# Kernel optimization log

Measured on AMD Instinct MI355X. Metric: run time of the kernel, lower is better.

The kernel has to match this reference:

```python
import jax, jax.numpy as jnp
import numpy as np

K = 12  # kNN neighbors (includes self, as in PyG knn(x, x, k))
EPS = 1e-5


def bn(h, g, b):
    # Training-mode BatchNorm over all axes except the last (feature) axis.
    ax = tuple(range(h.ndim - 1))
    m = h.mean(axis=ax, keepdims=True)
    v = h.var(axis=ax, keepdims=True)  # biased variance, as BN uses
    return g * (h - m) * jax.lax.rsqrt(v + EPS) + b


def edge_conv(x, W1, b1, g, be, W2, b2):
    # x: [B, N, C] -> [B, N, H]. Dynamic kNN graph in feature space per graph.
    d2 = jnp.sum(x * x, axis=-1)                                  # [B, N]
    dist = d2[:, :, None] + d2[:, None, :] - 2.0 * jnp.einsum('bic,bjc->bij', x, x)
    _, idx = jax.lax.top_k(-dist, K)                              # [B, N, K]
    xj = jnp.take_along_axis(x[:, None, :, :], idx[:, :, :, None], axis=2)  # [B,N,K,C]
    xi = jnp.broadcast_to(x[:, :, None, :], xj.shape)
    e = jnp.concatenate([xi, xj - xi], axis=-1)                   # [B,N,K,2C]
    h = jax.nn.relu(bn(jnp.einsum('bnkc,ch->bnkh', e, W1) + b1, g, be))
    h = jnp.einsum('bnkh,ho->bnko', h, W2) + b2
    return h.mean(axis=2)                                         # mean aggr over K


def setup_inputs() -> dict:
    key = jax.random.key(0)
    ks = jax.random.split(key, 8)
    B, N, C, H, Hf, O = 32, 1024, 3, 64, 32, 2
    s = 0.1
    return {
        'x': jax.random.normal(ks[0], (B, N, C), jnp.float32),
        'w0a': jax.random.normal(ks[1], (2 * C, H), jnp.float32) * s,
        'b0a': jnp.zeros((H,), jnp.float32),
        'g0': jnp.ones((H,), jnp.float32),
        'be0': jnp.zeros((H,), jnp.float32),
        'w0b': jax.random.normal(ks[2], (H, H), jnp.float32) * s,
        'b0b': jnp.zeros((H,), jnp.float32),
        'wa': jax.random.normal(ks[3], (3, 2 * H, H), jnp.float32) * s,
        'ba': jnp.zeros((3, H), jnp.float32),
        'ga': jnp.ones((3, H), jnp.float32),
        'bea': jnp.zeros((3, H), jnp.float32),
        'wb': jax.random.normal(ks[4], (3, H, H), jnp.float32) * s,
        'bb': jnp.zeros((3, H), jnp.float32),
        'wf1': jax.random.normal(ks[5], (H, Hf), jnp.float32) * s,
        'bf1': jnp.zeros((Hf,), jnp.float32),
        'gf': jnp.ones((Hf,), jnp.float32),
        'bef': jnp.zeros((Hf,), jnp.float32),
        'wf2': jax.random.normal(ks[6], (Hf, O), jnp.float32) * s,
        'bf2': jnp.zeros((O,), jnp.float32),
    }


def reference(x, w0a, b0a, g0, be0, w0b, b0b, wa, ba, ga, bea, wb, bb,
              wf1, bf1, gf, bef, wf2, bf2):
    # Layer 0: input channels = 3
    h = edge_conv(x, w0a, b0a, g0, be0, w0b, b0b)
    # Layers 1..3: input channels = hidden
    for i in range(3):
        h = edge_conv(h, wa[i], ba[i], ga[i], bea[i], wb[i], bb[i])
    pooled = h.mean(axis=1)  # global_mean_pool over nodes -> [B, H]
    z = jax.nn.relu(bn(pooled @ wf1 + bf1, gf, bef))
    return z @ wf2 + bf2     # [B, 2]
```

## Files before the change

### kernel.cpp

```cpp
#include <hip/hip_runtime.h>
#include <cstddef>

#define BATCH 32
#define NPTS  1024
#define K_NN  12
#define HID   64
#define BN_EPS 1e-5f

typedef short bf16x8 __attribute__((ext_vector_type(8)));
typedef float f32x4 __attribute__((ext_vector_type(4)));

template<int C>
__global__ __launch_bounds__(256) void d2_kernel(const float* __restrict__ x,
                                                 float* __restrict__ d2) {
  int gid = blockIdx.x * 256 + threadIdx.x;
  const float* xp = x + (size_t)gid * C;
  float s = 0.f;
#pragma unroll
  for (int c = 0; c < C; ++c) { float v = xp[c]; s = fmaf(v, v, s); }
  d2[gid] = s;
}

__device__ __forceinline__ unsigned long long dkey(float dval, int j) {
  int di = __float_as_int(dval);
  unsigned m = (unsigned)(di >> 31) | 0x80000000u;
  unsigned u = (unsigned)di ^ m;
  return ((unsigned long long)u << 32) | (unsigned)j;
}

__device__ __forceinline__ void cas_u64(unsigned long long &a, unsigned long long &b) {
  unsigned long long x = a, y = b;
  bool c = y < x;
  a = c ? y : x;
  b = c ? x : y;
}

__device__ __forceinline__ void sort16_u64(unsigned long long (&k)[16]) {
  cas_u64(k[0],k[1]);  cas_u64(k[2],k[3]);  cas_u64(k[4],k[5]);  cas_u64(k[6],k[7]);
  cas_u64(k[8],k[9]);  cas_u64(k[10],k[11]); cas_u64(k[12],k[13]); cas_u64(k[14],k[15]);
  cas_u64(k[0],k[2]);  cas_u64(k[1],k[3]);  cas_u64(k[4],k[6]);  cas_u64(k[5],k[7]);
  cas_u64(k[8],k[10]); cas_u64(k[9],k[11]); cas_u64(k[12],k[14]); cas_u64(k[13],k[15]);
  cas_u64(k[1],k[2]);  cas_u64(k[5],k[6]);  cas_u64(k[9],k[10]); cas_u64(k[13],k[14]);
  cas_u64(k[0],k[4]);  cas_u64(k[1],k[5]);  cas_u64(k[2],k[6]);  cas_u64(k[3],k[7]);
  cas_u64(k[8],k[12]); cas_u64(k[9],k[13]); cas_u64(k[10],k[14]); cas_u64(k[11],k[15]);
  cas_u64(k[2],k[4]);  cas_u64(k[3],k[5]);  cas_u64(k[10],k[12]); cas_u64(k[11],k[13]);
  cas_u64(k[1],k[2]);  cas_u64(k[3],k[4]);  cas_u64(k[5],k[6]);
  cas_u64(k[9],k[10]); cas_u64(k[11],k[12]); cas_u64(k[13],k[14]);
  cas_u64(k[0],k[8]);  cas_u64(k[1],k[9]);  cas_u64(k[2],k[10]); cas_u64(k[3],k[11]);
  cas_u64(k[4],k[12]); cas_u64(k[5],k[13]); cas_u64(k[6],k[14]); cas_u64(k[7],k[15]);
  cas_u64(k[4],k[8]);  cas_u64(k[5],k[9]);  cas_u64(k[6],k[10]); cas_u64(k[7],k[11]);
  cas_u64(k[2],k[4]);  cas_u64(k[3],k[5]);  cas_u64(k[6],k[8]);  cas_u64(k[7],k[9]);
  cas_u64(k[10],k[12]); cas_u64(k[11],k[13]);
  cas_u64(k[1],k[2]);  cas_u64(k[3],k[4]);  cas_u64(k[5],k[6]);  cas_u64(k[7],k[8]);
  cas_u64(k[9],k[10]); cas_u64(k[11],k[12]); cas_u64(k[13],k[14]);
}

__device__ __forceinline__ void merge12_u64(unsigned long long (&L)[12],
                                            const unsigned long long* S) {
#pragma unroll
  for (int i = 0; i < 12; ++i) {
    unsigned long long s = S[11 - i];
    L[i] = L[i] < s ? L[i] : s;
  }
  cas_u64(L[0],L[8]);  cas_u64(L[1],L[9]);  cas_u64(L[2],L[10]); cas_u64(L[3],L[11]);
  cas_u64(L[4],L[8]);  cas_u64(L[5],L[9]);  cas_u64(L[6],L[10]); cas_u64(L[7],L[11]);
  cas_u64(L[0],L[2]);  cas_u64(L[1],L[3]);  cas_u64(L[4],L[6]);  cas_u64(L[5],L[7]);
  cas_u64(L[8],L[10]); cas_u64(L[9],L[11]);
  cas_u64(L[0],L[1]);  cas_u64(L[2],L[3]);  cas_u64(L[4],L[5]);  cas_u64(L[6],L[7]);
  cas_u64(L[8],L[9]);  cas_u64(L[10],L[11]);
}

__global__ __launch_bounds__(512, 2) void knn64_mfma_kernel(
    const unsigned short* __restrict__ xh, const unsigned short* __restrict__ xm,
    const unsigned short* __restrict__ xl, const float* __restrict__ d2,
    int* __restrict__ idx) {
  const int b    = blockIdx.y;
  const int lane = threadIdx.x & 63;
  const int wv_u = __builtin_amdgcn_readfirstlane(threadIdx.x >> 6);
  const int i0   = blockIdx.x * 64;
  const size_t bbase = (size_t)b * NPTS;
  const float* d2b = d2 + bbase;

  constexpr int NE = 8 * K_NN;
  __shared__ __align__(16) char smem[60416];
  unsigned short* alds = (unsigned short*)smem;
  float* slab = (float*)(smem + 25600 + wv_u * 4352);
  unsigned long long* lk = (unsigned long long*)smem;

  const int qr = lane >> 4;
  const int lr = lane & 15;

  for (int it = threadIdx.x; it < 1536; it += 512) {
    const int row = it / 24, rem = it % 24, pl = rem >> 3, seg = rem & 7;
    const unsigned short* src = (pl == 0) ? xh : ((pl == 1) ? xm : xl);
    *(bf16x8*)(alds + row * 200 + pl * 64 + seg * 8) =
        *(const bf16x8*)(src + (bbase + i0 + row) * HID + seg * 8);
  }
  __syncthreads();

  unsigned long long L[K_NN];
#pragma unroll
  for (int k = 0; k < K_NN; ++k) L[k] = ~0ULL;

  const int j0 = wv_u * 128;

  bf16x8 Bh0, Bh1, Bm0, Bm1, Bl0, Bl1;
  {
    const size_t brow = (bbase + j0 + lr) * HID;
    Bh0 = *(const bf16x8*)(xh + brow + 0  + qr * 8);
    Bh1 = *(const bf16x8*)(xh + brow + 32 + qr * 8);
    Bm0 = *(const bf16x8*)(xm + brow + 0  + qr * 8);
    Bm1 = *(const bf16x8*)(xm + brow + 32 + qr * 8);
    Bl0 = *(const bf16x8*)(xl + brow + 0  + qr * 8);
    Bl1 = *(const bf16x8*)(xl + brow + 32 + qr * 8);
  }

#pragma unroll 1
  for (int chunk = 0; chunk < 8; ++chunk) {
    const int jb = j0 + chunk * 16;
    const bf16x8 bh0 = Bh0, bh1 = Bh1, bm0 = Bm0, bm1 = Bm1, bl0 = Bl0, bl1 = Bl1;

    f32x4 acc[4];
#pragma unroll
    for (int isub = 0; isub < 4; ++isub) acc[isub] = f32x4{0.f, 0.f, 0.f, 0.f};

#pragma unroll
    for (int isub = 0; isub < 4; ++isub) {
      const int ar = (isub * 16 + lr) * 200;
      bf16x8 Ah0 = *(const bf16x8*)(alds + ar + 0   + qr * 8);
      bf16x8 Ah1 = *(const bf16x8*)(alds + ar + 32  + qr * 8);
      bf16x8 Am0 = *(const bf16x8*)(alds + ar + 64  + qr * 8);
      bf16x8 Am1 = *(const bf16x8*)(alds + ar + 96  + qr * 8);
      bf16x8 Al0 = *(const bf16x8*)(alds + ar + 128 + qr * 8);
      bf16x8 Al1 = *(const bf16x8*)(alds + ar + 160 + qr * 8);
      f32x4 a = acc[isub];
      a = __builtin_amdgcn_mfma_f32_16x16x32_bf16(Ah0, bh0, a, 0, 0, 0);
      a = __builtin_amdgcn_mfma_f32_16x16x32_bf16(Ah1, bh1, a, 0, 0, 0);
      a = __builtin_amdgcn_mfma_f32_16x16x32_bf16(Ah0, bm0, a, 0, 0, 0);
      a = __builtin_amdgcn_mfma_f32_16x16x32_bf16(Ah1, bm1, a, 0, 0, 0);
      a = __builtin_amdgcn_mfma_f32_16x16x32_bf16(Am0, bh0, a, 0, 0, 0);
      a = __builtin_amdgcn_mfma_f32_16x16x32_bf16(Am1, bh1, a, 0, 0, 0);
      a = __builtin_amdgcn_mfma_f32_16x16x32_bf16(Ah0, bl0, a, 0, 0, 0);
      a = __builtin_amdgcn_mfma_f32_16x16x32_bf16(Ah1, bl1, a, 0, 0, 0);
      a = __builtin_amdgcn_mfma_f32_16x16x32_bf16(Al0, bh0, a, 0, 0, 0);
      a = __builtin_amdgcn_mfma_f32_16x16x32_bf16(Al1, bh1, a, 0, 0, 0);
      a = __builtin_amdgcn_mfma_f32_16x16x32_bf16(Am0, bm0, a, 0, 0, 0);
      a = __builtin_amdgcn_mfma_f32_16x16x32_bf16(Am1, bm1, a, 0, 0, 0);
      acc[isub] = a;
    }

    if (chunk < 7) {
      const size_t nrow = (bbase + jb + 16 + lr) * HID;
      Bh0 = *(const bf16x8*)(xh + nrow + 0  + qr * 8);
      Bh1 = *(const bf16x8*)(xh + nrow + 32 + qr * 8);
      Bm0 = *(const bf16x8*)(xm + nrow + 0  + qr * 8);
      Bm1 = *(const bf16x8*)(xm + nrow + 32 + qr * 8);
      Bl0 = *(const bf16x8*)(xl + nrow + 0  + qr * 8);
      Bl1 = *(const bf16x8*)(xl + nrow + 32 + qr * 8);
    }

#pragma unroll
    for (int isub = 0; isub < 4; ++isub)
#pragma unroll
      for (int r = 0; r < 4; ++r)
        slab[(isub * 16 + qr * 4 + r) * 17 + lr] = acc[isub][r];

    unsigned long long S[16];
#pragma unroll
    for (int jj = 0; jj < 16; ++jj) {
      const int j = jb + jj;
      const float dot = slab[lane * 17 + jj];
      const float dval = fmaf(-2.f, dot, d2b[j]);
      S[jj] = dkey(dval, j);
    }
    sort16_u64(S);
    merge12_u64(L, S);
  }

  __syncthreads();
#pragma unroll
  for (int k = 0; k < K_NN; ++k)
    lk[lane * (NE + 1) + wv_u * K_NN + k] = L[k];
  __syncthreads();

  if (wv_u == 0) {
#pragma unroll 1
    for (int w = 1; w < 8; ++w) {
      unsigned long long M[K_NN];
#pragma unroll
      for (int k = 0; k < K_NN; ++k) M[k] = lk[lane * (NE + 1) + w * K_NN + k];
      merge12_u64(L, M);
    }
    int* op = idx + ((size_t)b * NPTS + i0 + lane) * K_NN;
#pragma unroll
    for (int k = 0; k < K_NN; ++k) op[k] = (int)(unsigned)(L[k] & 0xFFFFFFFFu);
  }
}

__global__ __launch_bounds__(512, 2) void knn3_kernel(
    const float* __restrict__ x, const float* __restrict__ d2,
    int* __restrict__ idx) {
  const int b    = blockIdx.y;
  const int lane = threadIdx.x & 63;
  const int wv_u = __builtin_amdgcn_readfirstlane(threadIdx.x >> 6);
  const int i    = blockIdx.x * 64 + lane;
  const float* xb  = x  + (size_t)b * NPTS * 3;
  const float* d2b = d2 + (size_t)b * NPTS;

  constexpr int NE = 8 * K_NN;
  __shared__ __align__(16) unsigned long long lk[64 * (NE + 1)];

  float xi0 = xb[(size_t)i * 3 + 0];
  float xi1 = xb[(size_t)i * 3 + 1];
  float xi2v = xb[(size_t)i * 3 + 2];

  unsigned long long L[K_NN];
#pragma unroll
  for (int k = 0; k < K_NN; ++k) L[k] = ~0ULL;

  const int j0 = wv_u * 128;
#pragma unroll 1
  for (int ch = 0; ch < 8; ++ch) {
    unsigned long long S[16];
#pragma unroll
    for (int jj = 0; jj < 16; ++jj) {
      const int j = j0 + ch * 16 + jj;
      const float* xj = xb + (size_t)j * 3;
      const float d2j = d2b[j];
      float dot = fmaf(xi0, xj[0], 0.f);
      dot = fmaf(xi1, xj[1], dot);
      dot = fmaf(xi2v, xj[2], dot);
      S[jj] = dkey(fmaf(-2.f, dot, d2j), j);
    }
    sort16_u64(S);
    merge12_u64(L, S);
  }

#pragma unroll
  for (int k = 0; k < K_NN; ++k)
    lk[lane * (NE + 1) + wv_u * K_NN + k] = L[k];
  __syncthreads();

  if (wv_u == 0) {
#pragma unroll 1
    for (int w = 1; w < 8; ++w) {
      unsigned long long M[K_NN];
#pragma unroll
      for (int k = 0; k < K_NN; ++k) M[k] = lk[lane * (NE + 1) + w * K_NN + k];
      merge12_u64(L, M);
    }
    int* op = idx + ((size_t)b * NPTS + blockIdx.x * 64 + lane) * K_NN;
#pragma unroll
    for (int k = 0; k < K_NN; ++k) op[k] = (int)(unsigned)(L[k] & 0xFFFFFFFFu);
  }
}

__global__ __launch_bounds__(256) void rowgemm2_kernel(
    const float* __restrict__ X, const float* __restrict__ waL,
    const float* __restrict__ biasA,
    float* __restrict__ YA, float* __restrict__ YB) {
  __shared__ float wsa[HID * HID];
  __shared__ float wsb[HID * HID];
  for (int t = threadIdx.x; t < HID * HID; t += 256) {
    float wbv = waL[4096 + t];
    wsa[t] = waL[t] - wbv;
    wsb[t] = wbv;
  }
  __syncthreads();

  const int lane = threadIdx.x & 63;
  const int wv   = threadIdx.x >> 6;
  const int fq   = lane & 15;
  const int rg   = lane >> 4;
  const int r0   = blockIdx.x * 32 + wv * 8 + rg * 2;

  const float4* X4 = (const float4*)X;
  const float4* WA4 = (const float4*)wsa;
  const float4* WB4 = (const float4*)wsb;
  float aA0[4] = {0,0,0,0}, aA1[4] = {0,0,0,0};
  float aB0[4] = {0,0,0,0}, aB1[4] = {0,0,0,0};

#pragma unroll 2
  for (int cq = 0; cq < 16; ++cq) {
    float4 xa = X4[(size_t)r0 * 16 + cq];
    float4 xb_ = X4[(size_t)(r0 + 1) * 16 + cq];
    float ea[4] = {xa.x, xa.y, xa.z, xa.w};
    float eb[4] = {xb_.x, xb_.y, xb_.z, xb_.w};
#pragma unroll
    for (int d = 0; d < 4; ++d) {
      float4 wa4 = WA4[(cq * 4 + d) * 16 + fq];
      float4 wb4 = WB4[(cq * 4 + d) * 16 + fq];
      float wA[4] = {wa4.x, wa4.y, wa4.z, wa4.w};
      float wB[4] = {wb4.x, wb4.y, wb4.z, wb4.w};
#pragma unroll
      for (int k = 0; k < 4; ++k) {
        aA0[k] = fmaf(ea[d], wA[k], aA0[k]);
        aA1[k] = fmaf(eb[d], wA[k], aA1[k]);
        aB0[k] = fmaf(ea[d], wB[k], aB0[k]);
        aB1[k] = fmaf(eb[d], wB[k], aB1[k]);
      }
    }
  }
  float4 b4 = ((const float4*)biasA)[fq];
  float4 oA0{aA0[0] + b4.x, aA0[1] + b4.y, aA0[2] + b4.z, aA0[3] + b4.w};
  float4 oA1{aA1[0] + b4.x, aA1[1] + b4.y, aA1[2] + b4.z, aA1[3] + b4.w};
  float4 oB0{aB0[0], aB0[1], aB0[2], aB0[3]};
  float4 oB1{aB1[0], aB1[1], aB1[2], aB1[3]};
  ((float4*)YA)[(size_t)r0 * 16 + fq] = oA0;
  ((float4*)YA)[(size_t)(r0 + 1) * 16 + fq] = oA1;
  ((float4*)YB)[(size_t)r0 * 16 + fq] = oB0;
  ((float4*)YB)[(size_t)(r0 + 1) * 16 + fq] = oB1;
}

__global__ __launch_bounds__(256) void dual3_kernel(
    const float* __restrict__ x, const float* __restrict__ w0a,
    const float* __restrict__ b1,
    float* __restrict__ hxi, float* __restrict__ hxj) {
  __shared__ float Cs[3 * HID], Bs[3 * HID], bs[HID];
  for (int t = threadIdx.x; t < 3 * HID; t += 256) {
    float bv = w0a[192 + t];
    Cs[t] = w0a[t] - bv;
    Bs[t] = bv;
  }
  if (threadIdx.x < HID) bs[threadIdx.x] = b1[threadIdx.x];
  __syncthreads();

  const int lane = threadIdx.x & 63;
  const int wv   = __builtin_amdgcn_readfirstlane(threadIdx.x >> 6);
  const int node0 = blockIdx.x * 32;
#pragma unroll 1
  for (int it = 0; it < 8; ++it) {
    const int n = node0 + it * 4 + wv;
    const float* xr = x + (size_t)n * 3;
    float x0 = xr[0], x1 = xr[1], x2 = xr[2];
    float hi = bs[lane];
    hi = fmaf(x0, Cs[0 * HID + lane], hi);
    hi = fmaf(x1, Cs[1 * HID + lane], hi);
    hi = fmaf(x2, Cs[2 * HID + lane], hi);
    float hj = x0 * Bs[0 * HID + lane];
    hj = fmaf(x1, Bs[1 * HID + lane], hj);
    hj = fmaf(x2, Bs[2 * HID + lane], hj);
    hxi[(size_t)n * HID + lane] = hi;
    hxj[(size_t)n * HID + lane] = hj;
  }
}

__global__ __launch_bounds__(256) void egstats_kernel(
    const int* __restrict__ idx, const float* __restrict__ hxi,
    const float* __restrict__ hxj, float* __restrict__ partial) {
  const int lane = threadIdx.x & 63;
  const int wv   = __builtin_amdgcn_readfirstlane(threadIdx.x >> 6);
  const int node0 = blockIdx.x * 32;
  float s1 = 0.f, s2 = 0.f;

#pragma unroll 1
  for (int it = 0; it < 4; ++it) {
    const int n0 = node0 + it * 8 + wv;
    const int n1 = n0 + 4;
    const int bbase = (n0 >> 10) << 10;
    const int* ip0 = idx + (size_t)n0 * K_NN;
    const int* ip1 = idx + (size_t)n1 * K_NN;
    int j0[K_NN], j1[K_NN];
#pragma unroll
    for (int k = 0; k < K_NN; ++k) { j0[k] = ip0[k]; j1[k] = ip1[k]; }
    const float hv0 = hxi[(size_t)n0 * HID + lane];
    const float hv1 = hxi[(size_t)n1 * HID + lane];
    float v0[K_NN], v1[K_NN];
#pragma unroll
    for (int k = 0; k < K_NN; ++k) {
      v0[k] = hxj[(size_t)(bbase + j0[k]) * HID + lane];
      v1[k] = hxj[(size_t)(bbase + j1[k]) * HID + lane];
    }
#pragma unroll
    for (int k = 0; k < K_NN; ++k) {
      float h0 = hv0 + v0[k], h1 = hv1 + v1[k];
      s1 += h0 + h1;
      s2 = fmaf(h0, h0, s2); s2 = fmaf(h1, h1, s2);
    }
  }

  __shared__ float red[4][HID];
  red[wv][lane] = s1;
  __syncthreads();
  if (threadIdx.x < HID)
    partial[(size_t)blockIdx.x * 128 + lane] =
        (red[0][lane] + red[1][lane]) + (red[2][lane] + red[3][lane]);
  __syncthreads();
  red[wv][lane] = s2;
  __syncthreads();
  if (threadIdx.x < HID)
    partial[(size_t)blockIdx.x * 128 + 64 + lane] =
        (red[0][lane] + red[1][lane]) + (red[2][lane] + red[3][lane]);
}

__global__ __launch_bounds__(512) void bn_reduce_finalize_kernel(
    const float* __restrict__ g, const float* __restrict__ be,
    const float* __restrict__ partial, float* __restrict__ stats) {
  const int t   = threadIdx.x & 127;
  const int grp = threadIdx.x >> 7;
  float a0 = 0.f, a1 = 0.f, a2 = 0.f, a3 = 0.f;
  const int gb0 = grp * 256;
  for (int gb = gb0; gb < gb0 + 256; gb += 4) {
    a0 += partial[(size_t)(gb + 0) * 128 + t];
    a1 += partial[(size_t)(gb + 1) * 128 + t];
    a2 += partial[(size_t)(gb + 2) * 128 + t];
    a3 += partial[(size_t)(gb + 3) * 128 + t];
  }
  __shared__ float sm[4][128];
  sm[grp][t] = (a0 + a1) + (a2 + a3);
  __syncthreads();
  if (threadIdx.x < 128)
    sm[0][t] = (sm[0][t] + sm[1][t]) + (sm[2][t] + sm[3][t]);
  __syncthreads();
  if (threadIdx.x < HID) {
    const float inv_n = 1.f / (float)(BATCH * NPTS * K_NN);
    float m = sm[0][t] * inv_n;
    float v = sm[0][HID + t] * inv_n - m * m;
    float A = g[t] * rsqrtf(v + BN_EPS);
    stats[128 + t] = A;
    stats[192 + t] = be[t] - m * A;
  }
}

__global__ __launch_bounds__(256) void egapply_gemm_kernel(
    const int* __restrict__ idx, const float* __restrict__ hxi,
    const float* __restrict__ hxj, const float* __restrict__ stats,
    const float* __restrict__ W2, const float* __restrict__ b2,
    float* __restrict__ out, float* __restrict__ d2out,
    unsigned short* __restrict__ xsh, unsigned short* __restrict__ xsm,
    unsigned short* __restrict__ xsl) {
  __shared__ float w2s[HID * HID];
  __shared__ float red[32][HID];
  for (int t = threadIdx.x; t < HID * HID; t += 256) w2s[t] = W2[t];

  const int lane = threadIdx.x & 63;
  const int wv   = __builtin_amdgcn_readfirstlane(threadIdx.x >> 6);
  const int node0 = blockIdx.x * 32;
  const float A = stats[128 + lane], Bc = stats[192 + lane];

#pragma unroll 1
  for (int it = 0; it < 4; ++it) {
    const int n0 = node0 + it * 8 + wv;
    const int n1 = n0 + 4;
    const int bbase = (n0 >> 10) << 10;
    const int* ip0 = idx + (size_t)n0 * K_NN;
    const int* ip1 = idx + (size_t)n1 * K_NN;
    int j0[K_NN], j1[K_NN];
#pragma unroll
    for (int k = 0; k < K_NN; ++k) { j0[k] = ip0[k]; j1[k] = ip1[k]; }
    const float hv0 = hxi[(size_t)n0 * HID + lane];
    const float hv1 = hxi[(size_t)n1 * HID + lane];
    float v0[K_NN], v1[K_NN];
#pragma unroll
    for (int k = 0; k < K_NN; ++k) {
      v0[k] = hxj[(size_t)(bbase + j0[k]) * HID + lane];
      v1[k] = hxj[(size_t)(bbase + j1[k]) * HID + lane];
    }
    float a0 = 0.f, a1 = 0.f;
#pragma unroll
    for (int k = 0; k < K_NN; ++k) {
      a0 += fmaxf(fmaf(A, hv0 + v0[k], Bc), 0.f);
      a1 += fmaxf(fmaf(A, hv1 + v1[k], Bc), 0.f);
    }
    red[it * 8 + wv][lane] = a0;
    red[it * 8 + 4 + wv][lane] = a1;
  }
  __syncthreads();

  const float b2f = b2[lane];
  const float inv = 1.f / (float)K_NN;
#pragma unroll 2
  for (int p = 0; p < 8; ++p) {
    int rr = p * 4 + wv;
    float acc = 0.f;
#pragma unroll 8
    for (int h = 0; h < HID; ++h) acc = fmaf(red[rr][h], w2s[h * HID + lane], acc);
    float val = fmaf(acc, inv, b2f);
    const size_t o = (size_t)(node0 + rr) * HID + lane;
    out[o] = val;

    unsigned u = __float_as_uint(val);
    unsigned short hh = (unsigned short)((u + 0x7FFFu + ((u >> 16) & 1u)) >> 16);
    float r1 = val - __uint_as_float((unsigned)hh << 16);
    unsigned ur = __float_as_uint(r1);
    unsigned short mm = (unsigned short)((ur + 0x7FFFu + ((ur >> 16) & 1u)) >> 16);
    float r2 = r1 - __uint_as_float((unsigned)mm << 16);
    unsigned ur2 = __float_as_uint(r2);
    unsigned short ll = (unsigned short)((ur2 + 0x7FFFu + ((ur2 >> 16) & 1u)) >> 16);
    xsh[o] = hh; xsm[o] = mm; xsl[o] = ll;

    float sq = val * val;
#pragma unroll
    for (int off = 1; off < 64; off <<= 1) sq += __shfl_xor(sq, off, 64);
    if (lane == 0) d2out[node0 + rr] = sq;
  }
}

__global__ __launch_bounds__(256) void pool_kernel(const float* __restrict__ h,
                                                   float* __restrict__ pooled) {
  const int b = blockIdx.x;
  const int f = threadIdx.x & 63;
  const int gsz = threadIdx.x >> 6;
  __shared__ float red[4][HID];
  float s = 0.f;
  for (int n = gsz; n < NPTS; n += 4) s += h[((size_t)b * NPTS + n) * HID + f];
  red[gsz][f] = s;
  __syncthreads();
  if (threadIdx.x < HID)
    pooled[b * HID + f] = ((red[0][f] + red[1][f]) + (red[2][f] + red[3][f])) * (1.f / (float)NPTS);
}

__global__ __launch_bounds__(256) void head_kernel(const float* __restrict__ pooled,
    const float* __restrict__ wf1, const float* __restrict__ bf1,
    const float* __restrict__ gf, const float* __restrict__ bef,
    const float* __restrict__ wf2, const float* __restrict__ bf2,
    float* __restrict__ out) {
  __shared__ float pl[BATCH * HID];
  __shared__ float t[BATCH * 32];
  __shared__ float Ab[32], Bb[32];
  for (int i = threadIdx.x; i < BATCH * HID; i += 256) pl[i] = pooled[i];
  __syncthreads();
  for (int i = threadIdx.x; i < BATCH * 32; i += 256) {
    int s = i >> 5, f1 = i & 31;
    float acc = bf1[f1];
    for (int h = 0; h < HID; ++h) acc = fmaf(pl[s * HID + h], wf1[h * 32 + f1], acc);
    t[i] = acc;
  }
  __syncthreads();
  if (threadIdx.x < 32) {
    int f1 = threadIdx.x;
    float m = 0.f;
    for (int s = 0; s < BATCH; ++s) m += t[s * 32 + f1];
    m *= (1.f / (float)BATCH);
    float v = 0.f;
    for (int s = 0; s < BATCH; ++s) { float d = t[s * 32 + f1] - m; v = fmaf(d, d, v); }
    v *= (1.f / (float)BATCH);
    float A = gf[f1] * rsqrtf(v + BN_EPS);
    Ab[f1] = A; Bb[f1] = bef[f1] - m * A;
  }
  __syncthreads();
  for (int i = threadIdx.x; i < BATCH * 32; i += 256) {
    int f1 = i & 31;
    t[i] = fmaxf(fmaf(Ab[f1], t[i], Bb[f1]), 0.f);
  }
  __syncthreads();
  if (threadIdx.x < BATCH * 2) {
    int s = threadIdx.x >> 1, o = threadIdx.x & 1;
    float acc = bf2[o];
    for (int f1 = 0; f1 < 32; ++f1) acc = fmaf(t[s * 32 + f1], wf2[f1 * 2 + o], acc);
    out[s * 2 + o] = acc;
  }
}

extern "C" void kernel_launch(void* const* d_in, const int* in_sizes, int n_in,
                              void* d_out, int out_size, void* d_ws, size_t ws_size,
                              hipStream_t stream) {
  const float* x   = (const float*)d_in[0];
  const float* w0a = (const float*)d_in[1];
  const float* b0a = (const float*)d_in[2];
  const float* g0  = (const float*)d_in[3];
  const float* be0 = (const float*)d_in[4];
  const float* w0b = (const float*)d_in[5];
  const float* b0b = (const float*)d_in[6];
  const float* wa  = (const float*)d_in[7];
  const float* ba  = (const float*)d_in[8];
  const float* ga  = (const float*)d_in[9];
  const float* bea = (const float*)d_in[10];
  const float* wb  = (const float*)d_in[11];
  const float* bb  = (const float*)d_in[12];
  const float* wf1 = (const float*)d_in[13];
  const float* bf1 = (const float*)d_in[14];
  const float* gf  = (const float*)d_in[15];
  const float* bef = (const float*)d_in[16];
  const float* wf2 = (const float*)d_in[17];
  const float* bf2 = (const float*)d_in[18];

  float* ws = (float*)d_ws;
  const size_t HN = (size_t)BATCH * NPTS * HID;
  const size_t ROWS = (size_t)BATCH * NPTS;
  float* bufA    = ws;
  float* bufB    = bufA + HN;
  float* hxi     = bufB + HN;
  float* hxjb    = hxi + HN;
  int*   idxb    = (int*)(hxjb + HN);
  float* d2buf   = (float*)(idxb + ROWS * K_NN);
  float* stats   = d2buf + ROWS;
  float* partial = stats + 256;
  float* pooled  = partial + 1024 * 128;
  unsigned short* xsh = (unsigned short*)(pooled + 2048);
  unsigned short* xsm = xsh + HN;
  unsigned short* xsl = xsm + HN;

  d2_kernel<3><<<(int)(ROWS / 256), 256, 0, stream>>>(x, d2buf);
  knn3_kernel<<<dim3(16, BATCH), 512, 0, stream>>>(x, d2buf, idxb);
  dual3_kernel<<<1024, 256, 0, stream>>>(x, w0a, b0a, hxi, hxjb);
  egstats_kernel<<<1024, 256, 0, stream>>>(idxb, hxi, hxjb, partial);
  bn_reduce_finalize_kernel<<<1, 512, 0, stream>>>(g0, be0, partial, stats);
  egapply_gemm_kernel<<<1024, 256, 0, stream>>>(idxb, hxi, hxjb, stats, w0b, b0b,
                                                bufA, d2buf, xsh, xsm, xsl);

  const float* cur = bufA;
  float* nxt = bufB;
  for (int i = 0; i < 3; ++i) {
    knn64_mfma_kernel<<<dim3(16, BATCH), 512, 0, stream>>>(xsh, xsm, xsl, d2buf, idxb);
    rowgemm2_kernel<<<(int)(ROWS / 32), 256, 0, stream>>>(cur, wa + (size_t)i * 8192,
                                                          ba + i * HID, hxi, hxjb);
    egstats_kernel<<<1024, 256, 0, stream>>>(idxb, hxi, hxjb, partial);
    bn_reduce_finalize_kernel<<<1, 512, 0, stream>>>(ga + i * HID, bea + i * HID, partial, stats);
    egapply_gemm_kernel<<<1024, 256, 0, stream>>>(idxb, hxi, hxjb, stats,
                                                  wb + (size_t)i * 4096, bb + i * HID,
                                                  nxt, d2buf, xsh, xsm, xsl);
    const float* t = cur; cur = nxt; nxt = (float*)t;
  }

  pool_kernel<<<BATCH, 256, 0, stream>>>(cur, pooled);
  head_kernel<<<1, 256, 0, stream>>>(pooled, wf1, bf1, gf, bef, wf2, bf2, (float*)d_out);
}
```

Baseline: 608.4 us.

## Fuse BN edge-statistics pass into kNN kernels and parallelize final merge

The separate egstats kernel is removed and its BatchNorm sum/sum-of-squares accumulation moves into the tail of the knn3 and knn64 kernels. Neighbour indices stay in LDS and are reused directly, so idx is not re-read from global memory. The row GEMM producing hxi/hxj is reordered to run before kNN, and bn_reduce now reduces 512 partials instead of 1024. The final 8-way top-k merge becomes a two-level tree across two waves. This saves a launch and an idx round trip, but adds gather work and extra barriers to a kernel that runs only 512 blocks.

```diff
diff --git a/kernel.cpp b/kernel.cpp
--- a/kernel.cpp
+++ b/kernel.cpp
@@ -73,7 +73,9 @@
 __global__ __launch_bounds__(512, 2) void knn64_mfma_kernel(
     const unsigned short* __restrict__ xh, const unsigned short* __restrict__ xm,
     const unsigned short* __restrict__ xl, const float* __restrict__ d2,
-    int* __restrict__ idx) {
+    int* __restrict__ idx,
+    const float* __restrict__ hxi, const float* __restrict__ hxj,
+    float* __restrict__ partial) {
   const int b    = blockIdx.y;
   const int lane = threadIdx.x & 63;
   const int wv_u = __builtin_amdgcn_readfirstlane(threadIdx.x >> 6);
@@ -86,6 +88,9 @@
   unsigned short* alds = (unsigned short*)smem;
   float* slab = (float*)(smem + 25600 + wv_u * 4352);
   unsigned long long* lk = (unsigned long long*)smem;
+  int* jlds = (int*)(smem + 49664);
+  float* red1 = (float*)smem;
+  float* red2 = (float*)(smem + 2048);
 
   const int qr = lane >> 4;
   const int lr = lane & 15;
@@ -183,32 +188,100 @@
     lk[lane * (NE + 1) + wv_u * K_NN + k] = L[k];
   __syncthreads();
 
+  unsigned long long Lm[K_NN];
+  if (wv_u < 2) {
+    if (wv_u == 0) {
+#pragma unroll
+      for (int k = 0; k < K_NN; ++k) Lm[k] = L[k];
+    } else {
+#pragma unroll
+      for (int k = 0; k < K_NN; ++k) Lm[k] = lk[lane * (NE + 1) + 4 * K_NN + k];
+    }
+#pragma unroll 1
+    for (int w = 1; w < 4; ++w) {
+      unsigned long long M[K_NN];
+#pragma unroll
+      for (int k = 0; k < K_NN; ++k)
+        M[k] = lk[lane * (NE + 1) + (wv_u * 4 + w) * K_NN + k];
+      merge12_u64(Lm, M);
+    }
+  }
+  __syncthreads();
+  if (wv_u == 1) {
+#pragma unroll
+    for (int k = 0; k < K_NN; ++k) lk[lane * (NE + 1) + 4 * K_NN + k] = Lm[k];
+  }
+  __syncthreads();
   if (wv_u == 0) {
+    unsigned long long M[K_NN];
+#pragma unroll
+    for (int k = 0; k < K_NN; ++k) M[k] = lk[lane * (NE + 1) + 4 * K_NN + k];
+    merge12_u64(Lm, M);
+    int* op = idx + ((size_t)b * NPTS + i0 + lane) * K_NN;
+#pragma unroll
+    for (int k = 0; k < K_NN; ++k) {
+      int jv = (int)(unsigned)(Lm[k] & 0xFFFFFFFFu);
+      op[k] = jv;
+      jlds[lane * K_NN + k] = jv;
+    }
+  }
+  __syncthreads();
+
+  {
+    const float* hxib = hxi + (bbase + i0) * HID;
+    const float* hxjb = hxj + bbase * HID;
+    float s1 = 0.f, s2 = 0.f;
 #pragma unroll 1
-    for (int w = 1; w < 8; ++w) {
-      unsigned long long M[K_NN];
-#pragma unroll
-      for (int k = 0; k < K_NN; ++k) M[k] = lk[lane * (NE + 1) + w * K_NN + k];
-      merge12_u64(L, M);
-    }
-    int* op = idx + ((size_t)b * NPTS + i0 + lane) * K_NN;
-#pragma unroll
-    for (int k = 0; k < K_NN; ++k) op[k] = (int)(unsigned)(L[k] & 0xFFFFFFFFu);
+    for (int t = 0; t < 8; ++t) {
+      const int nl = wv_u * 8 + t;
+      const float hv = hxib[(size_t)nl * HID + lane];
+      int jj[K_NN];
+#pragma unroll
+      for (int k = 0; k < K_NN; ++k) jj[k] = jlds[nl * K_NN + k];
+      float v[K_NN];
+#pragma unroll
+      for (int k = 0; k < K_NN; ++k) v[k] = hxjb[(size_t)jj[k] * HID + lane];
+#pragma unroll
+      for (int k = 0; k < K_NN; ++k) {
+        float h = hv + v[k];
+        s1 += h;
+        s2 = fmaf(h, h, s2);
+      }
+    }
+    red1[wv_u * HID + lane] = s1;
+    red2[wv_u * HID + lane] = s2;
+  }
+  __syncthreads();
+  if (threadIdx.x < 128) {
+    const int f = threadIdx.x & 63;
+    const float* r = (threadIdx.x < 64) ? red1 : red2;
+    float a = 0.f;
+#pragma unroll
+    for (int w = 0; w < 8; ++w) a += r[w * HID + f];
+    partial[((size_t)b * 16 + blockIdx.x) * 128 + threadIdx.x] = a;
   }
 }
 
 __global__ __launch_bounds__(512, 2) void knn3_kernel(
     const float* __restrict__ x, const float* __restrict__ d2,
-    int* __restrict__ idx) {
+    int* __restrict__ idx,
+    const float* __restrict__ hxi, const float* __restrict__ hxj,
+    float* __restrict__ partial) {
   const int b    = blockIdx.y;
   const int lane = threadIdx.x & 63;
   const int wv_u = __builtin_amdgcn_readfirstlane(threadIdx.x >> 6);
-  const int i    = blockIdx.x * 64 + lane;
-  const float* xb  = x  + (size_t)b * NPTS * 3;
-  const float* d2b = d2 + (size_t)b * NPTS;
+  const int i0   = blockIdx.x * 64;
+  const int i    = i0 + lane;
+  const size_t bbase = (size_t)b * NPTS;
+  const float* xb  = x  + bbase * 3;
+  const float* d2b = d2 + bbase;
 
   constexpr int NE = 8 * K_NN;
-  __shared__ __align__(16) unsigned long long lk[64 * (NE + 1)];
+  __shared__ __align__(16) char smem[53248];
+  unsigned long long* lk = (unsigned long long*)smem;
+  int* jlds = (int*)(smem + 49664);
+  float* red1 = (float*)smem;
+  float* red2 = (float*)(smem + 2048);
 
   float xi0 = xb[(size_t)i * 3 + 0];
   float xi1 = xb[(size_t)i * 3 + 1];
@@ -241,17 +314,77 @@
     lk[lane * (NE + 1) + wv_u * K_NN + k] = L[k];
   __syncthreads();
 
+  unsigned long long Lm[K_NN];
+  if (wv_u < 2) {
+    if (wv_u == 0) {
+#pragma unroll
+      for (int k = 0; k < K_NN; ++k) Lm[k] = L[k];
+    } else {
+#pragma unroll
+      for (int k = 0; k < K_NN; ++k) Lm[k] = lk[lane * (NE + 1) + 4 * K_NN + k];
+    }
+#pragma unroll 1
+    for (int w = 1; w < 4; ++w) {
+      unsigned long long M[K_NN];
+#pragma unroll
+      for (int k = 0; k < K_NN; ++k)
+        M[k] = lk[lane * (NE + 1) + (wv_u * 4 + w) * K_NN + k];
+      merge12_u64(Lm, M);
+    }
+  }
+  __syncthreads();
+  if (wv_u == 1) {
+#pragma unroll
+    for (int k = 0; k < K_NN; ++k) lk[lane * (NE + 1) + 4 * K_NN + k] = Lm[k];
+  }
+  __syncthreads();
   if (wv_u == 0) {
+    unsigned long long M[K_NN];
+#pragma unroll
+    for (int k = 0; k < K_NN; ++k) M[k] = lk[lane * (NE + 1) + 4 * K_NN + k];
+    merge12_u64(Lm, M);
+    int* op = idx + ((size_t)b * NPTS + i0 + lane) * K_NN;
+#pragma unroll
+    for (int k = 0; k < K_NN; ++k) {
+      int jv = (int)(unsigned)(Lm[k] & 0xFFFFFFFFu);
+      op[k] = jv;
+      jlds[lane * K_NN + k] = jv;
+    }
+  }
+  __syncthreads();
+
+  {
+    const float* hxib = hxi + (bbase + i0) * HID;
+    const float* hxjb2 = hxj + bbase * HID;
+    float s1 = 0.f, s2 = 0.f;
 #pragma unroll 1
-    for (int w = 1; w < 8; ++w) {
-      unsigned long long M[K_NN];
-#pragma unroll
-      for (int k = 0; k < K_NN; ++k) M[k] = lk[lane * (NE + 1) + w * K_NN + k];
-      merge12_u64(L, M);
-    }
-    int* op = idx + ((size_t)b * NPTS + blockIdx.x * 64 + lane) * K_NN;
-#pragma unroll
-    for (int k = 0; k < K_NN; ++k) op[k] = (int)(unsigned)(L[k] & 0xFFFFFFFFu);
+    for (int t = 0; t < 8; ++t) {
+      const int nl = wv_u * 8 + t;
+      const float hv = hxib[(size_t)nl * HID + lane];
+      int jj[K_NN];
+#pragma unroll
+      for (int k = 0; k < K_NN; ++k) jj[k] = jlds[nl * K_NN + k];
+      float v[K_NN];
+#pragma unroll
+      for (int k = 0; k < K_NN; ++k) v[k] = hxjb2[(size_t)jj[k] * HID + lane];
+#pragma unroll
+      for (int k = 0; k < K_NN; ++k) {
+        float h = hv + v[k];
+        s1 += h;
+        s2 = fmaf(h, h, s2);
+      }
+    }
+    red1[wv_u * HID + lane] = s1;
+    red2[wv_u * HID + lane] = s2;
+  }
+  __syncthreads();
+  if (threadIdx.x < 128) {
+    const int f = threadIdx.x & 63;
+    const float* r = (threadIdx.x < 64) ? red1 : red2;
+    float a = 0.f;
+#pragma unroll
+    for (int w = 0; w < 8; ++w) a += r[w * HID + f];
+    partial[((size_t)b * 16 + blockIdx.x) * 128 + threadIdx.x] = a;
   }
 }
 
@@ -345,62 +478,14 @@
   }
 }
 
-__global__ __launch_bounds__(256) void egstats_kernel(
-    const int* __restrict__ idx, const float* __restrict__ hxi,
-    const float* __restrict__ hxj, float* __restrict__ partial) {
-  const int lane = threadIdx.x & 63;
-  const int wv   = __builtin_amdgcn_readfirstlane(threadIdx.x >> 6);
-  const int node0 = blockIdx.x * 32;
-  float s1 = 0.f, s2 = 0.f;
-
-#pragma unroll 1
-  for (int it = 0; it < 4; ++it) {
-    const int n0 = node0 + it * 8 + wv;
-    const int n1 = n0 + 4;
-    const int bbase = (n0 >> 10) << 10;
-    const int* ip0 = idx + (size_t)n0 * K_NN;
-    const int* ip1 = idx + (size_t)n1 * K_NN;
-    int j0[K_NN], j1[K_NN];
-#pragma unroll
-    for (int k = 0; k < K_NN; ++k) { j0[k] = ip0[k]; j1[k] = ip1[k]; }
-    const float hv0 = hxi[(size_t)n0 * HID + lane];
-    const float hv1 = hxi[(size_t)n1 * HID + lane];
-    float v0[K_NN], v1[K_NN];
-#pragma unroll
-    for (int k = 0; k < K_NN; ++k) {
-      v0[k] = hxj[(size_t)(bbase + j0[k]) * HID + lane];
-      v1[k] = hxj[(size_t)(bbase + j1[k]) * HID + lane];
-    }
-#pragma unroll
-    for (int k = 0; k < K_NN; ++k) {
-      float h0 = hv0 + v0[k], h1 = hv1 + v1[k];
-      s1 += h0 + h1;
-      s2 = fmaf(h0, h0, s2); s2 = fmaf(h1, h1, s2);
-    }
-  }
-
-  __shared__ float red[4][HID];
-  red[wv][lane] = s1;
-  __syncthreads();
-  if (threadIdx.x < HID)
-    partial[(size_t)blockIdx.x * 128 + lane] =
-        (red[0][lane] + red[1][lane]) + (red[2][lane] + red[3][lane]);
-  __syncthreads();
-  red[wv][lane] = s2;
-  __syncthreads();
-  if (threadIdx.x < HID)
-    partial[(size_t)blockIdx.x * 128 + 64 + lane] =
-        (red[0][lane] + red[1][lane]) + (red[2][lane] + red[3][lane]);
-}
-
 __global__ __launch_bounds__(512) void bn_reduce_finalize_kernel(
     const float* __restrict__ g, const float* __restrict__ be,
     const float* __restrict__ partial, float* __restrict__ stats) {
   const int t   = threadIdx.x & 127;
   const int grp = threadIdx.x >> 7;
   float a0 = 0.f, a1 = 0.f, a2 = 0.f, a3 = 0.f;
-  const int gb0 = grp * 256;
-  for (int gb = gb0; gb < gb0 + 256; gb += 4) {
+  const int gb0 = grp * 128;
+  for (int gb = gb0; gb < gb0 + 128; gb += 4) {
     a0 += partial[(size_t)(gb + 0) * 128 + t];
     a1 += partial[(size_t)(gb + 1) * 128 + t];
     a2 += partial[(size_t)(gb + 2) * 128 + t];
@@ -592,9 +677,8 @@
   unsigned short* xsl = xsm + HN;
 
   d2_kernel<3><<<(int)(ROWS / 256), 256, 0, stream>>>(x, d2buf);
-  knn3_kernel<<<dim3(16, BATCH), 512, 0, stream>>>(x, d2buf, idxb);
   dual3_kernel<<<1024, 256, 0, stream>>>(x, w0a, b0a, hxi, hxjb);
-  egstats_kernel<<<1024, 256, 0, stream>>>(idxb, hxi, hxjb, partial);
+  knn3_kernel<<<dim3(16, BATCH), 512, 0, stream>>>(x, d2buf, idxb, hxi, hxjb, partial);
   bn_reduce_finalize_kernel<<<1, 512, 0, stream>>>(g0, be0, partial, stats);
   egapply_gemm_kernel<<<1024, 256, 0, stream>>>(idxb, hxi, hxjb, stats, w0b, b0b,
                                                 bufA, d2buf, xsh, xsm, xsl);
@@ -602,10 +686,10 @@
   const float* cur = bufA;
   float* nxt = bufB;
   for (int i = 0; i < 3; ++i) {
-    knn64_mfma_kernel<<<dim3(16, BATCH), 512, 0, stream>>>(xsh, xsm, xsl, d2buf, idxb);
     rowgemm2_kernel<<<(int)(ROWS / 32), 256, 0, stream>>>(cur, wa + (size_t)i * 8192,
                                                           ba + i * HID, hxi, hxjb);
-    egstats_kernel<<<1024, 256, 0, stream>>>(idxb, hxi, hxjb, partial);
+    knn64_mfma_kernel<<<dim3(16, BATCH), 512, 0, stream>>>(xsh, xsm, xsl, d2buf, idxb,
+                                                           hxi, hxjb, partial);
     bn_reduce_finalize_kernel<<<1, 512, 0, stream>>>(ga + i * HID, bea + i * HID, partial, stats);
     egapply_gemm_kernel<<<1024, 256, 0, stream>>>(idxb, hxi, hxjb, stats,
                                                   wb + (size_t)i * 4096, bb + i * HID,
```

Result: faster. 580.0 us (-4.7%).
